# Optimization experiments

Hardware: AMD Instinct MI355X
Metric: run time of the kernel (lower is better)

## Reference

```python
import jax, jax.numpy as jnp
import numpy as np

B, N, K = 64, 512, 32   # batch, node_num, top_k
D = 64                  # dim == embed_dim == input_dim == out_channels
EPS = 1e-5
NEG_SLOPE = 0.2         # LeakyReLU slope in GraphLayer.message
NEG_INF = -1e9


def setup_inputs() -> dict:
    key = jax.random.key(0)
    ks = jax.random.split(key, 20)
    rn = lambda k, shp, s=1.0: jax.random.normal(k, shp, jnp.float32) * s
    return {
        "data": rn(ks[0], (B, N, D)),
        "org_edge_index": jax.random.randint(ks[1], (2, 1024), 0, N),
        "emb_table": rn(ks[2], (N, D)),                 # nn.Embedding(node_num, dim)
        "lin_W": rn(ks[3], (D, D), 1.0 / np.sqrt(D)),   # GraphLayer.lin (no bias)
        "att_i": rn(ks[4], (D,), 0.1),
        "att_j": rn(ks[5], (D,), 0.1),
        "att_em_i": rn(ks[6], (D,), 0.1),
        "att_em_j": rn(ks[7], (D,), 0.1),
        "gnn_bias": rn(ks[8], (D,), 0.1),
        "bn1_gamma": 1.0 + rn(ks[9], (D,), 0.1),
        "bn1_beta": rn(ks[10], (D,), 0.1),
        "bn1_mean": rn(ks[11], (D,), 0.1),
        "bn1_var": 0.5 + jax.random.uniform(ks[12], (D,), jnp.float32),
        "bno_gamma": 1.0 + rn(ks[13], (D,), 0.1),
        "bno_beta": rn(ks[14], (D,), 0.1),
        "bno_mean": rn(ks[15], (D,), 0.1),
        "bno_var": 0.5 + jax.random.uniform(ks[16], (D,), jnp.float32),
        "out_W": rn(ks[17], (1, D), 1.0 / np.sqrt(D)),  # OutLayer single Linear(dim,1)
        "out_b": rn(ks[18], (1,), 0.1),
    }


def _gdn_forward(data, emb_table, lin_W, att_i, att_j, att_em_i, att_em_j, gnn_bias,
                 bn1_gamma, bn1_beta, bn1_mean, bn1_var,
                 bno_gamma, bno_beta, bno_mean, bno_var, out_W, out_b):
    Bn, Nn, Fin = data.shape
    x = data.reshape(-1, Fin)                               # [B*N, Fin]

    # --- dynamic graph: cosine-sim topk on detached embedding ---
    w = jax.lax.stop_gradient(emb_table)                    # weights_arr = emb.detach()
    nrm = jnp.linalg.norm(w, axis=-1)
    cos = (w @ w.T) / (nrm[:, None] * nrm[None, :])         # [N, N]
    topk_idx = jax.lax.top_k(cos, K)[1]                     # [N, K]
    src0 = topk_idx.reshape(-1)                             # j (sources)
    dst0 = jnp.repeat(jnp.arange(Nn), K)                    # i (targets)
    valid0 = src0 != dst0                                   # remove_self_loops
    offs = (jnp.arange(Bn) * Nn)[:, None]
    src = (src0[None, :] + offs).reshape(-1)                # [B*N*K]
    dst = (dst0[None, :] + offs).reshape(-1)
    valid = jnp.tile(valid0, Bn)
    loops = jnp.arange(Bn * Nn)                             # add_self_loops
    src = jnp.concatenate([src, loops])
    dst = jnp.concatenate([dst, loops])
    valid = jnp.concatenate([valid, jnp.ones(Bn * Nn, bool)])

    # --- GraphLayer (heads=1, concat=False) ---
    xl = x @ lin_W.T                                        # [B*N, D]
    src_l = src % Nn                                        # embedding tiled over batch
    dst_l = dst % Nn
    a = (xl[dst] @ att_i + emb_table[dst_l] @ att_em_i
         + xl[src] @ att_j + emb_table[src_l] @ att_em_j)   # [E]
    a = jnp.where(a >= 0, a, NEG_SLOPE * a)                 # leaky_relu
    a = jnp.where(valid, a, NEG_INF)
    seg = Bn * Nn
    amax = jax.ops.segment_max(a, dst, num_segments=seg)    # stable softmax per target
    ex = jnp.where(valid, jnp.exp(a - amax[dst]), 0.0)
    denom = jax.ops.segment_sum(ex, dst, num_segments=seg)
    alpha = ex / denom[dst]                                 # [E]
    agg = jax.ops.segment_sum(xl[src] * alpha[:, None], dst, num_segments=seg) + gnn_bias

    # --- GNNLayer BN (eval) + relu ---
    h = (agg - bn1_mean) / jnp.sqrt(bn1_var + EPS) * bn1_gamma + bn1_beta
    h = jax.nn.relu(h).reshape(Bn, Nn, -1)

    # --- mul by node embedding, BN over channels (eval), relu, dropout(eval)=id ---
    h = h * emb_table[None]
    h = (h - bno_mean) / jnp.sqrt(bno_var + EPS) * bno_gamma + bno_beta
    h = jax.nn.relu(h)

    # --- OutLayer: single Linear(dim, 1) ---
    out = h @ out_W.T + out_b                               # [B, N, 1]
    return out.reshape(-1, Nn)                              # [B, N]


def reference(data, org_edge_index, emb_table, lin_W, att_i, att_j, att_em_i, att_em_j,
              gnn_bias, bn1_gamma, bn1_beta, bn1_mean, bn1_var,
              bno_gamma, bno_beta, bno_mean, bno_var, out_W, out_b):
    # org_edge_index is accepted but unused by GDN.forward (dynamic graph replaces it)
    del org_edge_index
    return _gdn_forward(data, emb_table, lin_W, att_i, att_j, att_em_i, att_em_j, gnn_bias,
                        bn1_gamma, bn1_beta, bn1_mean, bn1_var,
                        bno_gamma, bno_beta, bno_mean, bno_var, out_W, out_b)
```

## Files before the change

### kernel.cpp

```cpp
#include <hip/hip_runtime.h>
#include <hip/hip_bf16.h>
#include <math.h>

#define BB 64
#define NN 512
#define KK 32
#define DD 64
#define BN (BB*NN)
#define EPSC 1e-5f
#define NEG_SLOPE 0.2f
#define NEG_INF_A (-1e9f)

typedef unsigned long long ull;


__global__ void kA_cos(const float* __restrict__ emb, ull* __restrict__ keys) {
    __shared__ float4 As[256];
    __shared__ float4 Bs[1024];
    __shared__ float rsA[16];
    const int t = threadIdx.x;
    const int lane = t & 63;
    const int wave = t >> 6;
    const int bi = blockIdx.x >> 3;
    const int c0 = (blockIdx.x & 7) * 64;
    const float4* emb4 = (const float4*)emb;

    As[t] = emb4[bi*256 + t];
    #pragma unroll
    for (int p = 0; p < 4; ++p) {
        const int idx = t + 256*p;
        const int r = idx >> 4, q = idx & 15;
        Bs[(r<<4) | (q ^ (r & 15))] = emb4[c0*16 + idx];
    }
    __syncthreads();

    if (wave == 0) {
        const int r = lane >> 2, qq = lane & 3;
        float ss = 0.f;
        #pragma unroll
        for (int m = 0; m < 4; ++m) {
            const float4 a = As[r*16 + qq*4 + m];
            ss += a.x*a.x + a.y*a.y + a.z*a.z + a.w*a.w;
        }
        ss += __shfl_xor(ss, 1);
        ss += __shfl_xor(ss, 2);
        if (qq == 0) rsA[r] = rsqrtf(ss);
    }

    float4 Wr[16];
    float ssW = 0.f;
    #pragma unroll
    for (int q = 0; q < 16; ++q) {
        Wr[q] = Bs[(lane<<4) | (q ^ (lane & 15))];
        ssW += Wr[q].x*Wr[q].x + Wr[q].y*Wr[q].y + Wr[q].z*Wr[q].z + Wr[q].w*Wr[q].w;
    }
    const float rsW = rsqrtf(ssW);
    __syncthreads();

    #pragma unroll
    for (int r = 0; r < 4; ++r) {
        const int jr = wave*4 + r;
        float acc = 0.f;
        #pragma unroll
        for (int q = 0; q < 16; ++q) {
            const float4 a = As[jr*16 + q];
            const float4 w = Wr[q];
            acc += a.x*w.x + a.y*w.y + a.z*w.z + a.w*w.w;
        }
        const float c = acc * rsA[jr] * rsW;
        const int row = bi*16 + jr;
        const int col = c0 + lane;
        unsigned int u = __float_as_uint(c);
        u = (u & 0x80000000u) ? ~u : (u | 0x80000000u);
        keys[row*NN + col] = ((ull)u << 16) | (ull)(NN - 1 - col);
    }
}

__global__ void kB_rank(const ull* __restrict__ keys,
                        const float* __restrict__ emb,
                        const float* __restrict__ att_em_i,
                        const float* __restrict__ att_em_j,
                        const float* __restrict__ gnn_bias,
                        const float* __restrict__ g1, const float* __restrict__ b1,
                        const float* __restrict__ m1, const float* __restrict__ v1,
                        const float* __restrict__ go, const float* __restrict__ bo,
                        const float* __restrict__ mo, const float* __restrict__ vo,
                        int* __restrict__ topk,
                        float* __restrict__ ei, float* __restrict__ ej,
                        float* __restrict__ epi) {
    __shared__ ull ks[NN];
    const int i = blockIdx.x;
    const int t = threadIdx.x;
    ks[t] = keys[i*NN + t];

    if (t < DD) {
        const float e = emb[i*DD + t];
        float e1 = e * att_em_i[t];
        float e2 = e * att_em_j[t];
        #pragma unroll
        for (int m = 32; m > 0; m >>= 1) {
            e1 += __shfl_xor(e1, m);
            e2 += __shfl_xor(e2, m);
        }
        if (t == 0) { ei[i] = e1; ej[i] = e2; }
    }
    if (i == 0 && t >= 64 && t < 64 + DD) {
        const int d = t - 64;
        float s1 = g1[d] / sqrtf(v1[d] + EPSC);
        float B1 = (gnn_bias[d] - m1[d]) * s1 + b1[d];
        float so = go[d] / sqrtf(vo[d] + EPSC);
        float Bo = bo[d] - mo[d] * so;
        epi[d] = s1; epi[DD + d] = B1; epi[2*DD + d] = so; epi[3*DD + d] = Bo;
    }
    __syncthreads();
    const ull mykey = ks[t];
    int rank = 0;
    #pragma unroll 16
    for (int kk = 0; kk < NN; ++kk) rank += (ks[kk] > mykey) ? 1 : 0;
    if (rank < KK) topk[i*KK + rank] = t;
}

__global__ void k2_lin(const float* __restrict__ data,
                       const float* __restrict__ linW,
                       const float* __restrict__ att_i, const float* __restrict__ att_j,
                       const float* __restrict__ ei, const float* __restrict__ ej,
                       float* __restrict__ xl, float* __restrict__ si,
                       float* __restrict__ sj) {
    __shared__ float4 Ws[1024];
    __shared__ float4 xs[256];
    const int t = threadIdx.x;
    const int lane = t & 63;
    const int wave = t >> 6;
    const float4* W4 = (const float4*)linW;

    #pragma unroll
    for (int p = 0; p < 4; ++p) {
        const int idx = t + 256*p;
        const int r = idx >> 4, q = idx & 15;
        Ws[(r<<4) | (q ^ (r & 15))] = W4[idx];
    }
    xs[t] = ((const float4*)data)[blockIdx.x*256 + t];
    __syncthreads();

    float4 Wr[16];
    #pragma unroll
    for (int q = 0; q < 16; ++q) Wr[q] = Ws[(lane<<4) | (q ^ (lane & 15))];

    const int r0 = wave * 4;
    float acc0 = 0.f, acc1 = 0.f, acc2 = 0.f, acc3 = 0.f;
    #pragma unroll
    for (int q = 0; q < 16; ++q) {
        const float4 w = Wr[q];
        const float4 x0 = xs[(r0+0)*16 + q];
        const float4 x1 = xs[(r0+1)*16 + q];
        const float4 x2 = xs[(r0+2)*16 + q];
        const float4 x3 = xs[(r0+3)*16 + q];
        acc0 += x0.x*w.x + x0.y*w.y + x0.z*w.z + x0.w*w.w;
        acc1 += x1.x*w.x + x1.y*w.y + x1.z*w.z + x1.w*w.w;
        acc2 += x2.x*w.x + x2.y*w.y + x2.z*w.z + x2.w*w.w;
        acc3 += x3.x*w.x + x3.y*w.y + x3.z*w.z + x3.w*w.w;
    }

    const int vbase = blockIdx.x*16 + r0;
    xl[(vbase+0)*DD + lane] = acc0;
    xl[(vbase+1)*DD + lane] = acc1;
    xl[(vbase+2)*DD + lane] = acc2;
    xl[(vbase+3)*DD + lane] = acc3;

    const float ai = att_i[lane];
    const float aj = att_j[lane];
    float accs[4] = {acc0, acc1, acc2, acc3};
    #pragma unroll
    for (int r = 0; r < 4; ++r) {
        float pi = accs[r] * ai;
        float pj = accs[r] * aj;
        #pragma unroll
        for (int m = 32; m > 0; m >>= 1) {
            pi += __shfl_xor(pi, m);
            pj += __shfl_xor(pj, m);
        }
        if (lane == 0) {
            const int v = vbase + r;
            si[v] = pi + ei[v & (NN-1)];
            sj[v] = pj + ej[v & (NN-1)];
        }
    }
}

__global__ void k3_agg(const float* __restrict__ xl, const float* __restrict__ si,
                       const float* __restrict__ sj, const int* __restrict__ topk,
                       const float* __restrict__ emb,
                       const float* __restrict__ epi,
                       const float* __restrict__ outW, const float* __restrict__ outb,
                       float* __restrict__ out) {
    const int t = threadIdx.x;
    const int lane = t & 63;
    const int wave = t >> 6;
    const int bid = blockIdx.x;
    const int xcd = bid & 7;
    const int ixc = bid >> 3;
    const int b   = xcd + 8 * (ixc >> 7);
    const int i   = ((ixc & 127) << 2) + wave;
    const int tgt = b * NN + i;

    const bool isedge = (lane <= KK);
    int tk = i;
    bool valid = true;
    if (lane < KK) { tk = topk[i*KK + lane]; valid = (tk != i); }
    const int srcg = b * NN + tk;

    float a;
    if (isedge) {
        a = si[tgt] + sj[srcg];
        a = (a >= 0.f) ? a : NEG_SLOPE * a;
        if (!valid) a = NEG_INF_A;
    } else {
        a = -3.0e38f;
    }

    float amax = a;
    #pragma unroll
    for (int m = 32; m > 0; m >>= 1) amax = fmaxf(amax, __shfl_xor(amax, m));

    float ex = (isedge && valid) ? __expf(a - amax) : 0.f;
    float denom = ex;
    #pragma unroll
    for (int m = 32; m > 0; m >>= 1) denom += __shfl_xor(denom, m);
    const float alpha = ex * __builtin_amdgcn_rcpf(denom);

    const int c4 = lane & 15;
    const int e4 = lane >> 4;
    const float4* xl4 = (const float4*)xl;

    float al[9];
    int   off[9];
    #pragma unroll
    for (int m = 0; m < 8; ++m) {
        const int kk = 4*m + e4;
        al[m]  = __shfl(alpha, kk);
        off[m] = __shfl(srcg, kk)*16 + c4;
    }
    const float alpha32 = __shfl(alpha, KK);
    const int   srcg32  = __shfl(srcg, KK);
    al[8]  = (e4 == 0) ? alpha32 : 0.f;
    off[8] = srcg32*16 + c4;

    float4 xv[9];
    #pragma unroll
    for (int m = 0; m < 9; ++m) xv[m] = xl4[off[m]];

    float4 acc = make_float4(0.f, 0.f, 0.f, 0.f);
    #pragma unroll
    for (int m = 0; m < 9; ++m) {
        acc.x += al[m]*xv[m].x; acc.y += al[m]*xv[m].y;
        acc.z += al[m]*xv[m].z; acc.w += al[m]*xv[m].w;
    }

    #pragma unroll
    for (int m = 16; m <= 32; m <<= 1) {
        acc.x += __shfl_xor(acc.x, m);
        acc.y += __shfl_xor(acc.y, m);
        acc.z += __shfl_xor(acc.z, m);
        acc.w += __shfl_xor(acc.w, m);
    }

    const float4* epi4 = (const float4*)epi;
    const float4 s1 = epi4[c4];
    const float4 B1 = epi4[16 + c4];
    const float4 so = epi4[32 + c4];
    const float4 Bo = epi4[48 + c4];
    const float4 em = ((const float4*)emb)[i*16 + c4];
    const float4 w4 = ((const float4*)outW)[c4];
    float4 h;
    h.x = fmaxf(acc.x*s1.x + B1.x, 0.f) * em.x;
    h.y = fmaxf(acc.y*s1.y + B1.y, 0.f) * em.y;
    h.z = fmaxf(acc.z*s1.z + B1.z, 0.f) * em.z;
    h.w = fmaxf(acc.w*s1.w + B1.w, 0.f) * em.w;
    h.x = fmaxf(h.x*so.x + Bo.x, 0.f);
    h.y = fmaxf(h.y*so.y + Bo.y, 0.f);
    h.z = fmaxf(h.z*so.z + Bo.z, 0.f);
    h.w = fmaxf(h.w*so.w + Bo.w, 0.f);
    float p = h.x*w4.x + h.y*w4.y + h.z*w4.z + h.w*w4.w;
    p += __shfl_xor(p, 1);
    p += __shfl_xor(p, 2);
    p += __shfl_xor(p, 4);
    p += __shfl_xor(p, 8);
    if (lane == 0) out[tgt] = p + outb[0];
}

extern "C" void kernel_launch(void* const* d_in, const int* in_sizes, int n_in,
                              void* d_out, int out_size, void* d_ws, size_t ws_size,
                              hipStream_t stream) {
    (void)in_sizes; (void)n_in; (void)out_size; (void)ws_size;
    const float* data   = (const float*)d_in[0];
    const float* emb    = (const float*)d_in[2];
    const float* linW   = (const float*)d_in[3];
    const float* att_i  = (const float*)d_in[4];
    const float* att_j  = (const float*)d_in[5];
    const float* attemi = (const float*)d_in[6];
    const float* attemj = (const float*)d_in[7];
    const float* gbias  = (const float*)d_in[8];
    const float* g1     = (const float*)d_in[9];
    const float* b1     = (const float*)d_in[10];
    const float* m1     = (const float*)d_in[11];
    const float* v1     = (const float*)d_in[12];
    const float* go     = (const float*)d_in[13];
    const float* bo     = (const float*)d_in[14];
    const float* mo     = (const float*)d_in[15];
    const float* vo     = (const float*)d_in[16];
    const float* outW   = (const float*)d_in[17];
    const float* outb   = (const float*)d_in[18];
    float* out = (float*)d_out;

    char* ws = (char*)d_ws;
    float* ei   = (float*)(ws + 0);
    float* ej   = (float*)(ws + 4096);
    float* epi  = (float*)(ws + 8192);
    int*   topk = (int*)  (ws + 16384);
    float* si   = (float*)(ws + 81920);
    float* sj   = (float*)(ws + 212992);
    float* xl   = (float*)(ws + 344064);
    ull*   keys = (ull*)  (ws + 344064);

    kA_cos<<<256, 256, 0, stream>>>(emb, keys);
    kB_rank<<<NN, NN, 0, stream>>>(keys, emb, attemi, attemj, gbias,
                                   g1, b1, m1, v1, go, bo, mo, vo,
                                   topk, ei, ej, epi);
    k2_lin<<<BN/16, 256, 0, stream>>>(data, linW, att_i, att_j, ei, ej,
                                      xl, si, sj);
    k3_agg<<<BN/4, 256, 0, stream>>>(xl, si, sj, topk, emb, epi,
                                     outW, outb, out);
}
```

Baseline: 137.0 us.

## Fuse cosine-similarity and top-k rank kernels into one per-row kernel

Measured after the change: 145.2 us. 1.06x slower.

```diff
diff --git a/kernel.cpp b/kernel.cpp
--- a/kernel.cpp
+++ b/kernel.cpp
@@ -14,110 +14,85 @@
 typedef unsigned long long ull;
 
 
-__global__ void kA_cos(const float* __restrict__ emb, ull* __restrict__ keys) {
-    __shared__ float4 As[256];
-    __shared__ float4 Bs[1024];
-    __shared__ float rsA[16];
+__global__ void kTop(const float* __restrict__ emb,
+                     const float* __restrict__ att_em_i,
+                     const float* __restrict__ att_em_j,
+                     const float* __restrict__ gnn_bias,
+                     const float* __restrict__ g1, const float* __restrict__ b1,
+                     const float* __restrict__ m1, const float* __restrict__ v1,
+                     const float* __restrict__ go, const float* __restrict__ bo,
+                     const float* __restrict__ mo, const float* __restrict__ vo,
+                     int* __restrict__ topk,
+                     float* __restrict__ ei, float* __restrict__ ej,
+                     float* __restrict__ epi) {
+    __shared__ float4 As[16];
+    __shared__ float4 Bs[4096];
+    __shared__ ull keys[NN];
+    const int i = blockIdx.x;
     const int t = threadIdx.x;
-    const int lane = t & 63;
-    const int wave = t >> 6;
-    const int bi = blockIdx.x >> 3;
-    const int c0 = (blockIdx.x & 7) * 64;
     const float4* emb4 = (const float4*)emb;
 
-    As[t] = emb4[bi*256 + t];
-    #pragma unroll
-    for (int p = 0; p < 4; ++p) {
-        const int idx = t + 256*p;
-        const int r = idx >> 4, q = idx & 15;
-        Bs[(r<<4) | (q ^ (r & 15))] = emb4[c0*16 + idx];
-    }
-    __syncthreads();
-
-    if (wave == 0) {
-        const int r = lane >> 2, qq = lane & 3;
-        float ss = 0.f;
+    if (t < 16) As[t] = emb4[i*16 + t];
+
+    for (int half = 0; half < 2; ++half) {
+        const int c0 = half * 256;
         #pragma unroll
-        for (int m = 0; m < 4; ++m) {
-            const float4 a = As[r*16 + qq*4 + m];
-            ss += a.x*a.x + a.y*a.y + a.z*a.z + a.w*a.w;
-        }
-        ss += __shfl_xor(ss, 1);
-        ss += __shfl_xor(ss, 2);
-        if (qq == 0) rsA[r] = rsqrtf(ss);
-    }
-
-    float4 Wr[16];
-    float ssW = 0.f;
-    #pragma unroll
-    for (int q = 0; q < 16; ++q) {
-        Wr[q] = Bs[(lane<<4) | (q ^ (lane & 15))];
-        ssW += Wr[q].x*Wr[q].x + Wr[q].y*Wr[q].y + Wr[q].z*Wr[q].z + Wr[q].w*Wr[q].w;
-    }
-    const float rsW = rsqrtf(ssW);
-    __syncthreads();
-
-    #pragma unroll
-    for (int r = 0; r < 4; ++r) {
-        const int jr = wave*4 + r;
-        float acc = 0.f;
+        for (int p = 0; p < 16; ++p) {
+            const int idx = t + 256*p;
+            const int r = idx >> 4, q = idx & 15;
+            Bs[(r<<4) | (q ^ (r & 15))] = emb4[c0*16 + idx];
+        }
+        __syncthreads();
+
+        float dot = 0.f, ssW = 0.f, ssA = 0.f;
         #pragma unroll
         for (int q = 0; q < 16; ++q) {
-            const float4 a = As[jr*16 + q];
-            const float4 w = Wr[q];
-            acc += a.x*w.x + a.y*w.y + a.z*w.z + a.w*w.w;
-        }
-        const float c = acc * rsA[jr] * rsW;
-        const int row = bi*16 + jr;
-        const int col = c0 + lane;
+            const float4 w = Bs[(t<<4) | (q ^ (t & 15))];
+            const float4 a = As[q];
+            dot += a.x*w.x + a.y*w.y + a.z*w.z + a.w*w.w;
+            ssW += w.x*w.x + w.y*w.y + w.z*w.z + w.w*w.w;
+            ssA += a.x*a.x + a.y*a.y + a.z*a.z + a.w*a.w;
+        }
+        const float c = dot * rsqrtf(ssA) * rsqrtf(ssW);
+        const int col = c0 + t;
         unsigned int u = __float_as_uint(c);
         u = (u & 0x80000000u) ? ~u : (u | 0x80000000u);
-        keys[row*NN + col] = ((ull)u << 16) | (ull)(NN - 1 - col);
-    }
-}
-
-__global__ void kB_rank(const ull* __restrict__ keys,
-                        const float* __restrict__ emb,
-                        const float* __restrict__ att_em_i,
-                        const float* __restrict__ att_em_j,
-                        const float* __restrict__ gnn_bias,
-                        const float* __restrict__ g1, const float* __restrict__ b1,
-                        const float* __restrict__ m1, const float* __restrict__ v1,
-                        const float* __restrict__ go, const float* __restrict__ bo,
-                        const float* __restrict__ mo, const float* __restrict__ vo,
-                        int* __restrict__ topk,
-                        float* __restrict__ ei, float* __restrict__ ej,
-                        float* __restrict__ epi) {
-    __shared__ ull ks[NN];
-    const int i = blockIdx.x;
-    const int t = threadIdx.x;
-    ks[t] = keys[i*NN + t];
-
-    if (t < DD) {
-        const float e = emb[i*DD + t];
-        float e1 = e * att_em_i[t];
-        float e2 = e * att_em_j[t];
-        #pragma unroll
-        for (int m = 32; m > 0; m >>= 1) {
-            e1 += __shfl_xor(e1, m);
-            e2 += __shfl_xor(e2, m);
-        }
-        if (t == 0) { ei[i] = e1; ej[i] = e2; }
-    }
-    if (i == 0 && t >= 64 && t < 64 + DD) {
-        const int d = t - 64;
-        float s1 = g1[d] / sqrtf(v1[d] + EPSC);
-        float B1 = (gnn_bias[d] - m1[d]) * s1 + b1[d];
-        float so = go[d] / sqrtf(vo[d] + EPSC);
-        float Bo = bo[d] - mo[d] * so;
-        epi[d] = s1; epi[DD + d] = B1; epi[2*DD + d] = so; epi[3*DD + d] = Bo;
-    }
-    __syncthreads();
-    const ull mykey = ks[t];
-    int rank = 0;
-    #pragma unroll 16
-    for (int kk = 0; kk < NN; ++kk) rank += (ks[kk] > mykey) ? 1 : 0;
-    if (rank < KK) topk[i*KK + rank] = t;
+        keys[col] = ((ull)u << 16) | (ull)(NN - 1 - col);
+        __syncthreads();
+    }
+
+    for (int jj = t; jj < NN; jj += 256) {
+        const ull mykey = keys[jj];
+        int rank = 0;
+        #pragma unroll 16
+        for (int kk = 0; kk < NN; ++kk) rank += (keys[kk] > mykey) ? 1 : 0;
+        if (rank < KK) topk[i*KK + rank] = jj;
+    }
+
+    if (i == 0) {
+        const float4* ami = (const float4*)att_em_i;
+        const float4* amj = (const float4*)att_em_j;
+        for (int cc = t; cc < NN; cc += 256) {
+            float e1 = 0.f, e2 = 0.f;
+            #pragma unroll
+            for (int q = 0; q < 16; ++q) {
+                const float4 e  = emb4[cc*16 + q];
+                const float4 a1 = ami[q];
+                const float4 a2 = amj[q];
+                e1 += e.x*a1.x + e.y*a1.y + e.z*a1.z + e.w*a1.w;
+                e2 += e.x*a2.x + e.y*a2.y + e.z*a2.z + e.w*a2.w;
+            }
+            ei[cc] = e1; ej[cc] = e2;
+        }
+        if (t < DD) {
+            const int d = t;
+            float s1 = g1[d] / sqrtf(v1[d] + EPSC);
+            float B1 = (gnn_bias[d] - m1[d]) * s1 + b1[d];
+            float so = go[d] / sqrtf(vo[d] + EPSC);
+            float Bo = bo[d] - mo[d] * so;
+            epi[d] = s1; epi[DD + d] = B1; epi[2*DD + d] = so; epi[3*DD + d] = Bo;
+        }
+    }
 }
 
 __global__ void k2_lin(const float* __restrict__ data,
@@ -320,12 +295,10 @@
     float* si   = (float*)(ws + 81920);
     float* sj   = (float*)(ws + 212992);
     float* xl   = (float*)(ws + 344064);
-    ull*   keys = (ull*)  (ws + 344064);
-
-    kA_cos<<<256, 256, 0, stream>>>(emb, keys);
-    kB_rank<<<NN, NN, 0, stream>>>(keys, emb, attemi, attemj, gbias,
-                                   g1, b1, m1, v1, go, bo, mo, vo,
-                                   topk, ei, ej, epi);
+
+    kTop<<<NN, 256, 0, stream>>>(emb, attemi, attemj, gbias,
+                                 g1, b1, m1, v1, go, bo, mo, vo,
+                                 topk, ei, ej, epi);
     k2_lin<<<BN/16, 256, 0, stream>>>(data, linW, att_i, att_j, ei, ej,
                                       xl, si, sj);
     k3_agg<<<BN/4, 256, 0, stream>>>(xl, si, sj, topk, emb, epi,
```
